# Optimization experiments

Measured on AMD Instinct MI355X. Metric: run time of the kernel, lower is better.

Reference implementation:

```python
import jax, jax.numpy as jnp
import numpy as np

N, E, D_IN, H1, C1, D_OUT = 50000, 800000, 384, 4, 64, 5
D_HID = H1 * C1  # 256, input to layer 2


def setup_inputs() -> dict:
    key = jax.random.key(0)
    ks = jax.random.split(key, 12)

    def lin(k, i, o):
        return (jax.random.normal(k, (i, o), jnp.float32) / np.sqrt(i)).astype(jnp.float32)

    inp = {
        "x": jax.random.normal(ks[0], (N, D_IN), jnp.float32),
        "edge_index": jax.random.randint(ks[1], (2, E), 0, N, jnp.int32),
        # layer 1: TransformerConv(384 -> 64, heads=4, concat=True)
        "Wq1": lin(ks[2], D_IN, H1 * C1), "bq1": jnp.zeros((H1 * C1,), jnp.float32),
        "Wk1": lin(ks[3], D_IN, H1 * C1), "bk1": jnp.zeros((H1 * C1,), jnp.float32),
        "Wv1": lin(ks[4], D_IN, H1 * C1), "bv1": jnp.zeros((H1 * C1,), jnp.float32),
        "Ws1": lin(ks[5], D_IN, H1 * C1), "bs1": jnp.zeros((H1 * C1,), jnp.float32),
        # layer 2: TransformerConv(256 -> 5, heads=1, concat=False)
        "Wq2": lin(ks[6], D_HID, D_OUT), "bq2": jnp.zeros((D_OUT,), jnp.float32),
        "Wk2": lin(ks[7], D_HID, D_OUT), "bk2": jnp.zeros((D_OUT,), jnp.float32),
        "Wv2": lin(ks[8], D_HID, D_OUT), "bv2": jnp.zeros((D_OUT,), jnp.float32),
        "Ws2": lin(ks[9], D_HID, D_OUT), "bs2": jnp.zeros((D_OUT,), jnp.float32),
    }
    return inp


def _segment_softmax(logits, dst, n):
    # logits: [E, H] grouped by destination node
    m = jax.ops.segment_max(logits, dst, num_segments=n)
    m = jnp.where(jnp.isfinite(m), m, 0.0)
    e = jnp.exp(logits - m[dst])
    s = jax.ops.segment_sum(e, dst, num_segments=n)
    return e / (s[dst] + 1e-16)


def _transformer_conv(x, src, dst, Wq, bq, Wk, bk, Wv, bv, Ws, bs, heads, out_ch, concat):
    n = x.shape[0]
    q = (x @ Wq + bq).reshape(n, heads, out_ch)
    k = (x @ Wk + bk).reshape(n, heads, out_ch)
    v = (x @ Wv + bv).reshape(n, heads, out_ch)
    # per-edge attention logits: q_i . k_j / sqrt(C)   [E, H]
    logits = jnp.einsum('ehc,ehc->eh', q[dst], k[src]) / jnp.sqrt(jnp.float32(out_ch))
    alpha = _segment_softmax(logits, dst, n)          # [E, H]
    msg = v[src] * alpha[:, :, None]                  # [E, H, C]
    out = jax.ops.segment_sum(msg, dst, num_segments=n)  # [N, H, C]
    out = out.reshape(n, heads * out_ch) if concat else out.mean(axis=1)
    # root skip connection (root_weight=True default in PyG)
    return out + (x @ Ws + bs)


def reference(x, edge_index, Wq1, bq1, Wk1, bk1, Wv1, bv1, Ws1, bs1,
              Wq2, bq2, Wk2, bk2, Wv2, bv2, Ws2, bs2):
    src, dst = edge_index[0], edge_index[1]
    h = _transformer_conv(x, src, dst, Wq1, bq1, Wk1, bk1, Wv1, bv1, Ws1, bs1,
                          H1, C1, True)
    h = jax.nn.relu(h)
    out = _transformer_conv(h, src, dst, Wq2, bq2, Wk2, bk2, Wv2, bv2, Ws2, bs2,
                            1, D_OUT, False)
    return out
```

## Files before the change

kernel.cpp:

```cpp
#include <hip/hip_runtime.h>
#include <hip/hip_bf16.h>

#define N_NODES 50000
#define N_EDGES 800000
#define NPAD    50048
#define SCAN_B  196

typedef __attribute__((ext_vector_type(8))) short bf16x8;
typedef __attribute__((ext_vector_type(8))) unsigned short u16x8;
typedef __attribute__((ext_vector_type(4))) float f32x4;

__device__ __forceinline__ unsigned short f2bf(float f) {
  union { float f; unsigned u; } x; x.f = f;
  unsigned r = x.u + 0x7fffu + ((x.u >> 16) & 1u);
  return (unsigned short)(r >> 16);
}
__device__ __forceinline__ float bf2f(unsigned short u) {
  union { unsigned u; float f; } x; x.u = ((unsigned)u) << 16;
  return x.f;
}
__device__ __forceinline__ unsigned char enc8v(float v) {
  float t = fminf(fmaxf(fmaf(v, 16.f, 128.5f), 0.f), 255.f);
  return (unsigned char)(int)t;
}
__device__ __forceinline__ char enc8k(float v) {
  float t = fminf(fmaxf(v * 16.f, -127.f), 127.f);
  return (char)(int)floorf(t + 0.5f);
}
__device__ __forceinline__ char enc8q(float v) {
  float t = fminf(fmaxf(v * 24.f, -127.f), 127.f);
  return (char)(int)floorf(t + 0.5f);
}

__device__ __forceinline__ int dot4i8(int a, int b, int c) {
#if __has_builtin(__builtin_amdgcn_sdot4)
  return __builtin_amdgcn_sdot4(a, b, c, false);
#else
  int r = c;
  r += (int)(char)(a) * (int)(char)(b);
  r += (int)(char)(a >> 8) * (int)(char)(b >> 8);
  r += (int)(char)(a >> 16) * (int)(char)(b >> 16);
  r += (int)(char)(a >> 24) * (int)(char)(b >> 24);
  return r;
#endif
}

__device__ __forceinline__ void gload16(const unsigned short* g, unsigned short* l) {
  __builtin_amdgcn_global_load_lds(
      (const __attribute__((address_space(1))) unsigned int*)g,
      (__attribute__((address_space(3))) unsigned int*)l, 16, 0, 0);
}

__global__ void hist_kernel(const int* __restrict__ dst, int* __restrict__ counts, int E) {
  int e = blockIdx.x * 256 + threadIdx.x;
  if (e < E) atomicAdd(&counts[dst[e]], 1);
}

__global__ __launch_bounds__(256) void scan1_kernel(const int* __restrict__ counts,
                                                    int* __restrict__ tmp, int* __restrict__ bsum, int n) {
  __shared__ int sm[256];
  int i = blockIdx.x * 256 + threadIdx.x;
  int v = (i < n) ? counts[i] : 0;
  sm[threadIdx.x] = v;
  __syncthreads();
  for (int off = 1; off < 256; off <<= 1) {
    int t = (threadIdx.x >= off) ? sm[threadIdx.x - off] : 0;
    __syncthreads();
    sm[threadIdx.x] += t;
    __syncthreads();
  }
  if (i < n) tmp[i] = sm[threadIdx.x] - v;
  if (threadIdx.x == 255) bsum[blockIdx.x] = sm[255];
}

__global__ __launch_bounds__(256) void scan2_kernel(const int* __restrict__ bsum,
                                                    int* __restrict__ bbase, int nb) {
  __shared__ int sm[256];
  int v = (threadIdx.x < nb) ? bsum[threadIdx.x] : 0;
  sm[threadIdx.x] = v;
  __syncthreads();
  for (int off = 1; off < 256; off <<= 1) {
    int t = (threadIdx.x >= off) ? sm[threadIdx.x - off] : 0;
    __syncthreads();
    sm[threadIdx.x] += t;
    __syncthreads();
  }
  if (threadIdx.x < nb) bbase[threadIdx.x] = sm[threadIdx.x] - v;
}

__global__ __launch_bounds__(256) void scan3_kernel(const int* __restrict__ tmp,
                                                    const int* __restrict__ bbase,
                                                    int* __restrict__ offsets, int* __restrict__ cursor,
                                                    int n, int E) {
  int i = blockIdx.x * 256 + threadIdx.x;
  if (i < n) {
    int o = tmp[i] + bbase[blockIdx.x];
    offsets[i] = o;
    cursor[i] = o;
  }
  if (i == 0) offsets[n] = E;
}

__global__ void scatter_kernel(const int* __restrict__ src, const int* __restrict__ dst,
                               int* __restrict__ cursor, int* __restrict__ csr_src, int E) {
  int e = blockIdx.x * 256 + threadIdx.x;
  if (e < E) {
    int pos = atomicAdd(&cursor[dst[e]], 1);
    csr_src[pos] = src[e];
  }
}

__global__ void convert_x_kernel(const float* __restrict__ x, unsigned short* __restrict__ xb,
                                 int total_real, int total_pad) {
  long i = ((long)blockIdx.x * 256 + threadIdx.x) * 8;
  if (i >= total_pad) return;
  u16x8 o;
  if (i < total_real) {
    float4 v0 = *(const float4*)&x[i];
    float4 v1 = *(const float4*)&x[i + 4];
    o[0] = (short)f2bf(v0.x); o[1] = (short)f2bf(v0.y);
    o[2] = (short)f2bf(v0.z); o[3] = (short)f2bf(v0.w);
    o[4] = (short)f2bf(v1.x); o[5] = (short)f2bf(v1.y);
    o[6] = (short)f2bf(v1.z); o[7] = (short)f2bf(v1.w);
  } else {
    o = (u16x8)0;
  }
  *(u16x8*)&xb[i] = o;
}

__global__ void pack_w1_kernel(const float* __restrict__ Wq, const float* __restrict__ Wk,
                               const float* __restrict__ Wv, const float* __restrict__ Ws,
                               const float* __restrict__ bq, const float* __restrict__ bk,
                               const float* __restrict__ bv, const float* __restrict__ bs_,
                               unsigned short* __restrict__ wbt, float* __restrict__ bias1) {
  int idx = blockIdx.x * 256 + threadIdx.x;
  if (idx >= 1024 * 384) return;
  int n = idx / 384, k = idx - n * 384;
  int blk = n >> 8, cc = n & 255;
  const float* W = (blk == 0) ? Wq : (blk == 1) ? Wk : (blk == 2) ? Wv : Ws;
  wbt[idx] = f2bf(W[(long)k * 256 + cc]);
  if (k == 0) {
    const float* b = (blk == 0) ? bq : (blk == 1) ? bk : (blk == 2) ? bv : bs_;
    bias1[n] = b[cc];
  }
}

__global__ void pack_w2_kernel(const float* __restrict__ Wq, const float* __restrict__ Wk,
                               const float* __restrict__ Wv, const float* __restrict__ Ws,
                               const float* __restrict__ bq, const float* __restrict__ bk,
                               const float* __restrict__ bv, const float* __restrict__ bs_,
                               unsigned short* __restrict__ w2bt, float* __restrict__ bias2) {
  int idx = blockIdx.x * 256 + threadIdx.x;
  if (idx >= 32 * 256) return;
  int c = idx >> 8, p = idx & 255;
  unsigned short o = 0;
  if (c < 20) {
    int blk = c / 5, cc = c - blk * 5;
    int tch = (p & 0xC0) + (p & 3) * 16 + ((p & 63) >> 2);
    const float* W = (blk == 0) ? Wq : (blk == 1) ? Wk : (blk == 2) ? Wv : Ws;
    o = f2bf(W[(long)tch * 5 + cc]);
    if (p == 0) {
      const float* b = (blk == 0) ? bq : (blk == 1) ? bk : (blk == 2) ? bv : bs_;
      bias2[c] = b[cc];
    }
  }
  w2bt[idx] = o;
}

__global__ __launch_bounds__(512) void gemm1_kernel(
    const unsigned short* __restrict__ xb, const unsigned short* __restrict__ wbt,
    const float* __restrict__ bias,
    char* __restrict__ qb8, unsigned char* __restrict__ kvb,
    unsigned short* __restrict__ s1b) {
  __shared__ unsigned short As[2][128 * 32];
  __shared__ unsigned short Bs[2][256 * 32];
  int bid = blockIdx.x;
  int grp = bid >> 5, bl = bid & 31;
  int mx = grp * 8 + (bl & 7);
  int y = bl >> 3;
  if (mx >= NPAD / 128) return;
  int tid = threadIdx.x;
  long m0 = (long)mx * 128;
  int n0 = y * 256;
  int w = tid >> 6, l = tid & 63;
  int wr = (w >> 2) * 64, wc = (w & 3) * 64;
  int lr = l & 15, c0 = l >> 4;
  int sw = (lr ^ (lr >> 2)) & 3;
  int swoff = (c0 ^ sw) * 8;
  f32x4 acc[4][4] = {};
  int rs = tid >> 2, ss = tid & 3;
  int fa = (rs ^ (rs >> 2)) & 3;
  int fb1 = ((rs + 128) ^ ((rs + 128) >> 2)) & 3;
  const unsigned short* gA  = xb + (m0 + rs) * 384 + ((ss ^ fa) * 8);
  const unsigned short* gB0 = wbt + (long)(n0 + rs) * 384 + ((ss ^ fa) * 8);
  const unsigned short* gB1 = wbt + (long)(n0 + rs + 128) * 384 + ((ss ^ fb1) * 8);
  gload16(gA, &As[0][tid * 8]);
  gload16(gB0, &Bs[0][tid * 8]);
  gload16(gB1, &Bs[0][4096 + tid * 8]);
  __syncthreads();
  for (int kt = 0; kt < 12; ++kt) {
    int b = kt & 1;
    if (kt < 11) {
      int ko = (kt + 1) * 32;
      gload16(gA + ko, &As[b ^ 1][tid * 8]);
      gload16(gB0 + ko, &Bs[b ^ 1][tid * 8]);
      gload16(gB1 + ko, &Bs[b ^ 1][4096 + tid * 8]);
    }
    bf16x8 af[4], bfv[4];
#pragma unroll
    for (int mf = 0; mf < 4; ++mf) af[mf] = *(const bf16x8*)&As[b][(wr + mf * 16 + lr) * 32 + swoff];
#pragma unroll
    for (int nf = 0; nf < 4; ++nf) bfv[nf] = *(const bf16x8*)&Bs[b][(wc + nf * 16 + lr) * 32 + swoff];
#pragma unroll
    for (int mf = 0; mf < 4; ++mf)
#pragma unroll
      for (int nf = 0; nf < 4; ++nf)
        acc[mf][nf] = __builtin_amdgcn_mfma_f32_16x16x32_bf16(af[mf], bfv[nf], acc[mf][nf], 0, 0, 0);
    __syncthreads();
  }
  float bv[4];
#pragma unroll
  for (int nf = 0; nf < 4; ++nf) bv[nf] = bias[n0 + wc + nf * 16 + lr];
  int pos = wc + lr * 4;
#pragma unroll
  for (int mf = 0; mf < 4; ++mf) {
#pragma unroll
    for (int i = 0; i < 4; ++i) {
      long row = m0 + wr + mf * 16 + c0 * 4 + i;
      float v0 = acc[mf][0][i] + bv[0];
      float v1 = acc[mf][1][i] + bv[1];
      float v2 = acc[mf][2][i] + bv[2];
      float v3 = acc[mf][3][i] + bv[3];
      if (y == 0) {
        char4 st; st.x = enc8q(v0); st.y = enc8q(v1); st.z = enc8q(v2); st.w = enc8q(v3);
        *(char4*)&qb8[row * 256 + pos] = st;
      } else if (y == 1) {
        char4 st; st.x = enc8k(v0); st.y = enc8k(v1); st.z = enc8k(v2); st.w = enc8k(v3);
        *(char4*)&kvb[row * 512 + pos] = st;
      } else if (y == 2) {
        uchar4 st; st.x = enc8v(v0); st.y = enc8v(v1); st.z = enc8v(v2); st.w = enc8v(v3);
        *(uchar4*)&kvb[row * 512 + 256 + pos] = st;
      } else {
        ushort4 st; st.x = f2bf(v0); st.y = f2bf(v1); st.z = f2bf(v2); st.w = f2bf(v3);
        *(ushort4*)&s1b[row * 256 + pos] = st;
      }
    }
  }
}

__global__ __launch_bounds__(256) void agg1_kernel(
    const char* __restrict__ qb8, const unsigned char* __restrict__ kvb,
    unsigned short* s1b,
    const int* __restrict__ offsets, const int* __restrict__ csr_src) {
  int w = threadIdx.x >> 6, l = threadIdx.x & 63;
  int g = l >> 4;
  int sub = l & 15;
  for (int n = blockIdx.x * 4 + w; n < N_NODES; n += gridDim.x * 4) {
    int4 qi = *(const int4*)&qb8[(long)n * 256 + sub * 16];
    float acc[16] = {};
    float se = 0.f;
    int i0 = offsets[n], i1 = offsets[n + 1];
#define VACC(E, W, B) \
    acc[(B) + 0] = fmaf(E, (float)((W) & 0xffu), acc[(B) + 0]); \
    acc[(B) + 1] = fmaf(E, (float)(((W) >> 8) & 0xffu), acc[(B) + 1]); \
    acc[(B) + 2] = fmaf(E, (float)(((W) >> 16) & 0xffu), acc[(B) + 2]); \
    acc[(B) + 3] = fmaf(E, (float)((W) >> 24), acc[(B) + 3]);
    for (int i = i0; i < i1; i += 8) {
      int ia = i + g, ib = i + 4 + g;
      int sa = csr_src[ia < i1 ? ia : i1 - 1];
      int sb = csr_src[ib < i1 ? ib : i1 - 1];
      const char* ba = (const char*)kvb + (long)sa * 512 + sub * 16;
      const char* bb = (const char*)kvb + (long)sb * 512 + sub * 16;
      int4 ka = *(const int4*)ba;
      int4 kw = *(const int4*)bb;
      uint4 va = *(const uint4*)(ba + 256);
      uint4 vw = *(const uint4*)(bb + 256);
      int da = 0, db = 0;
      da = dot4i8(qi.x, ka.x, da); da = dot4i8(qi.y, ka.y, da);
      da = dot4i8(qi.z, ka.z, da); da = dot4i8(qi.w, ka.w, da);
      db = dot4i8(qi.x, kw.x, db); db = dot4i8(qi.y, kw.y, db);
      db = dot4i8(qi.z, kw.z, db); db = dot4i8(qi.w, kw.w, db);
      da += __shfl_xor(da, 1); da += __shfl_xor(da, 2);
      db += __shfl_xor(db, 1); db += __shfl_xor(db, 2);
      float ea = (ia < i1) ? __expf((float)da * (1.f / 3072.f)) : 0.f;
      float eb = (ib < i1) ? __expf((float)db * (1.f / 3072.f)) : 0.f;
      se += ea + eb;
      VACC(ea, va.x, 0) VACC(ea, va.y, 4) VACC(ea, va.z, 8) VACC(ea, va.w, 12)
      VACC(eb, vw.x, 0) VACC(eb, vw.y, 4) VACC(eb, vw.z, 8) VACC(eb, vw.w, 12)
    }
#undef VACC
#pragma unroll
    for (int j = 0; j < 16; ++j) {
      acc[j] += __shfl_xor(acc[j], 16);
      acc[j] += __shfl_xor(acc[j], 32);
    }
    se += __shfl_xor(se, 16);
    se += __shfl_xor(se, 32);
    if (g == 0) {
      float inv = (se > 0.f) ? 1.0f / se : 0.f;
      float bias = (se > 0.f) ? -8.0f : 0.f;
      long ob = (long)n * 256 + sub * 16;
      u16x8 sv0 = *(const u16x8*)&s1b[ob];
      u16x8 sv1 = *(const u16x8*)&s1b[ob + 8];
      u16x8 h0, h1;
#pragma unroll
      for (int j = 0; j < 8; ++j) {
        float v0 = fmaf(acc[j] * inv, 0.0625f, bias);
        float v1 = fmaf(acc[8 + j] * inv, 0.0625f, bias);
        h0[j] = (short)f2bf(fmaxf(v0 + bf2f((unsigned short)sv0[j]), 0.f));
        h1[j] = (short)f2bf(fmaxf(v1 + bf2f((unsigned short)sv1[j]), 0.f));
      }
      *(u16x8*)&s1b[ob] = h0;
      *(u16x8*)&s1b[ob + 8] = h1;
    }
  }
}

__global__ __launch_bounds__(256) void lin2_kernel(const unsigned short* __restrict__ hb,
                                                   const unsigned short* __restrict__ w2bt,
                                                   const float* __restrict__ bias2,
                                                   float* __restrict__ qs2, float* __restrict__ kv2) {
  __shared__ unsigned short Bs2[32 * 264];
  __shared__ float bsh[32];
  for (int i = threadIdx.x; i < 32 * 32; i += 256) {
    int r = i >> 5, cc = i & 31;
    *(u16x8*)&Bs2[r * 264 + cc * 8] = *(const u16x8*)&w2bt[r * 256 + cc * 8];
  }
  if (threadIdx.x < 32) bsh[threadIdx.x] = (threadIdx.x < 20) ? bias2[threadIdx.x] : 0.f;
  __syncthreads();
  int w = threadIdx.x >> 6, l = threadIdx.x & 63;
  long row0 = (long)blockIdx.x * 128 + w * 32;
  int lr = l & 15, c0 = l >> 4;
  f32x4 acc[2][2] = {};
  for (int kk = 0; kk < 8; ++kk) {
    int koff = kk * 32 + c0 * 8;
    bf16x8 af[2], bfv[2];
    af[0] = *(const bf16x8*)&hb[(row0 + lr) * 256 + koff];
    af[1] = *(const bf16x8*)&hb[(row0 + 16 + lr) * 256 + koff];
    bfv[0] = *(const bf16x8*)&Bs2[lr * 264 + koff];
    bfv[1] = *(const bf16x8*)&Bs2[(16 + lr) * 264 + koff];
#pragma unroll
    for (int mf = 0; mf < 2; ++mf)
#pragma unroll
      for (int nf = 0; nf < 2; ++nf)
        acc[mf][nf] = __builtin_amdgcn_mfma_f32_16x16x32_bf16(af[mf], bfv[nf], acc[mf][nf], 0, 0, 0);
  }
#pragma unroll
  for (int mf = 0; mf < 2; ++mf) {
#pragma unroll
    for (int nf = 0; nf < 2; ++nf) {
      int col = nf * 16 + lr;
#pragma unroll
      for (int i = 0; i < 4; ++i) {
        long n = row0 + mf * 16 + c0 * 4 + i;
        float v = acc[mf][nf][i] + bsh[col];
        if (col < 5) qs2[n * 12 + col] = v;
        else if (col < 15) kv2[n * 12 + (col - 5)] = v;
        else if (col < 20) qs2[n * 12 + (col - 10)] = v;
      }
    }
  }
}

__global__ void agg2_kernel(const float* __restrict__ qs2, const float* __restrict__ kv2,
                            const int* __restrict__ offsets, const int* __restrict__ csr_src,
                            float* __restrict__ out) {
  int n = blockIdx.x * 256 + threadIdx.x;
  if (n >= N_NODES) return;
  const float* bn = &qs2[(long)n * 12];
  const float is5 = 0.4472135954999579f;
  float q[5], acc[5] = {0, 0, 0, 0, 0}, se = 0.f;
#pragma unroll
  for (int c = 0; c < 5; ++c) q[c] = bn[c] * is5;
  int i0 = offsets[n], i1 = offsets[n + 1];
  for (int i = i0; i < i1; ++i) {
    int s = csr_src[i];
    const float4* ps = (const float4*)&kv2[(long)s * 12];
    float4 A = ps[0], B = ps[1], C = ps[2];
    float lg = q[0] * A.x + q[1] * A.y + q[2] * A.z + q[3] * A.w + q[4] * B.x;
    float ee = __expf(lg);
    se += ee;
    acc[0] += ee * B.y; acc[1] += ee * B.z; acc[2] += ee * B.w;
    acc[3] += ee * C.x; acc[4] += ee * C.y;
  }
  float inv = 1.f / (se + 1e-16f);
#pragma unroll
  for (int c = 0; c < 5; ++c) out[(long)n * 5 + c] = acc[c] * inv + bn[5 + c];
}

extern "C" void kernel_launch(void* const* d_in, const int* in_sizes, int n_in,
                              void* d_out, int out_size, void* d_ws, size_t ws_size,
                              hipStream_t stream) {
  (void)in_sizes; (void)n_in; (void)out_size; (void)ws_size;
  const float* x   = (const float*)d_in[0];
  const int* eidx  = (const int*)d_in[1];
  const int* esrc  = eidx;
  const int* edst  = eidx + N_EDGES;
  const float* Wq1 = (const float*)d_in[2];  const float* bq1 = (const float*)d_in[3];
  const float* Wk1 = (const float*)d_in[4];  const float* bk1 = (const float*)d_in[5];
  const float* Wv1 = (const float*)d_in[6];  const float* bv1 = (const float*)d_in[7];
  const float* Ws1 = (const float*)d_in[8];  const float* bs1 = (const float*)d_in[9];
  const float* Wq2 = (const float*)d_in[10]; const float* bq2 = (const float*)d_in[11];
  const float* Wk2 = (const float*)d_in[12]; const float* bk2 = (const float*)d_in[13];
  const float* Wv2 = (const float*)d_in[14]; const float* bv2 = (const float*)d_in[15];
  const float* Ws2 = (const float*)d_in[16]; const float* bs2 = (const float*)d_in[17];

  char* p = (char*)d_ws;
  auto take = [&](size_t bytes) { char* r = p; p += (bytes + 255) & ~(size_t)255; return r; };
  unsigned short* xb  = (unsigned short*)take((size_t)NPAD * 384 * 2);
  unsigned short* wbt = (unsigned short*)take((size_t)1024 * 384 * 2);
  float* bias1        = (float*)take(1024 * 4);
  char* qb8           = (char*)take((size_t)NPAD * 256);
  unsigned char* kvb  = (unsigned char*)take((size_t)NPAD * 512);
  unsigned short* s1b = (unsigned short*)take((size_t)NPAD * 256 * 2);
  unsigned short* w2bt = (unsigned short*)take(32 * 256 * 2);
  float* bias2        = (float*)take(32 * 4);
  float* qs2          = (float*)take((size_t)NPAD * 12 * 4);
  float* kv2          = (float*)take((size_t)NPAD * 12 * 4);
  int* counts         = (int*)take((size_t)N_NODES * 4);
  int* offsets        = (int*)take((size_t)(N_NODES + 1) * 4);
  int* cursor         = (int*)take((size_t)N_NODES * 4);
  int* csr_src        = (int*)take((size_t)N_EDGES * 4);
  int* scan_tmp       = (int*)take((size_t)N_NODES * 4);
  int* scan_bsum      = (int*)take(256 * 4);
  int* scan_bbase     = (int*)take(256 * 4);

  hipMemsetAsync(counts, 0, (size_t)N_NODES * 4, stream);
  hist_kernel<<<(N_EDGES + 255) / 256, 256, 0, stream>>>(edst, counts, N_EDGES);
  scan1_kernel<<<SCAN_B, 256, 0, stream>>>(counts, scan_tmp, scan_bsum, N_NODES);
  scan2_kernel<<<1, 256, 0, stream>>>(scan_bsum, scan_bbase, SCAN_B);
  scan3_kernel<<<SCAN_B, 256, 0, stream>>>(scan_tmp, scan_bbase, offsets, cursor, N_NODES, N_EDGES);
  scatter_kernel<<<(N_EDGES + 255) / 256, 256, 0, stream>>>(esrc, edst, cursor, csr_src, N_EDGES);
  convert_x_kernel<<<(NPAD * 384 / 8 + 255) / 256, 256, 0, stream>>>(x, xb, N_NODES * 384, NPAD * 384);
  pack_w1_kernel<<<(1024 * 384 + 255) / 256, 256, 0, stream>>>(Wq1, Wk1, Wv1, Ws1, bq1, bk1, bv1, bs1, wbt, bias1);
  pack_w2_kernel<<<(32 * 256 + 255) / 256, 256, 0, stream>>>(Wq2, Wk2, Wv2, Ws2, bq2, bk2, bv2, bs2, w2bt, bias2);
  gemm1_kernel<<<((NPAD / 128 + 7) / 8) * 32, 512, 0, stream>>>(xb, wbt, bias1, qb8, kvb, s1b);
  agg1_kernel<<<2048, 256, 0, stream>>>(qb8, kvb, s1b, offsets, csr_src);
  lin2_kernel<<<NPAD / 128, 256, 0, stream>>>(s1b, w2bt, bias2, qs2, kv2);
  agg2_kernel<<<(N_NODES + 255) / 256, 256, 0, stream>>>(qs2, kv2, offsets, csr_src, (float*)d_out);
}
```

Before: 279.7 us.

## Fuse fp32-to-bf16 conversion of x into GEMM1 and prefetch edges in agg1

Removes the separate x conversion kernel and its bf16 staging buffer. GEMM1 now reads fp32 x rows straight from global memory into registers and packs them to bf16 MFMA fragments, so only the weight tile goes through LDS, which drops from double to single buffering. agg1 gains a one-batch software prefetch of neighbour K/V loads and an early path for nodes with no incoming edges. This saves a full read and write pass over x, but GEMM1 loses its global-to-LDS overlap, and each x element is now read four times, once per N-column block.

```diff
diff --git a/kernel.cpp b/kernel.cpp
--- a/kernel.cpp
+++ b/kernel.cpp
@@ -18,6 +18,9 @@
 __device__ __forceinline__ float bf2f(unsigned short u) {
   union { unsigned u; float f; } x; x.u = ((unsigned)u) << 16;
   return x.f;
+}
+__device__ __forceinline__ unsigned pkbf(float lo, float hi) {
+  return ((unsigned)f2bf(hi) << 16) | f2bf(lo);
 }
 __device__ __forceinline__ unsigned char enc8v(float v) {
   float t = fminf(fmaxf(fmaf(v, 16.f, 128.5f), 0.f), 255.f);
@@ -108,24 +111,6 @@
     int pos = atomicAdd(&cursor[dst[e]], 1);
     csr_src[pos] = src[e];
   }
-}
-
-__global__ void convert_x_kernel(const float* __restrict__ x, unsigned short* __restrict__ xb,
-                                 int total_real, int total_pad) {
-  long i = ((long)blockIdx.x * 256 + threadIdx.x) * 8;
-  if (i >= total_pad) return;
-  u16x8 o;
-  if (i < total_real) {
-    float4 v0 = *(const float4*)&x[i];
-    float4 v1 = *(const float4*)&x[i + 4];
-    o[0] = (short)f2bf(v0.x); o[1] = (short)f2bf(v0.y);
-    o[2] = (short)f2bf(v0.z); o[3] = (short)f2bf(v0.w);
-    o[4] = (short)f2bf(v1.x); o[5] = (short)f2bf(v1.y);
-    o[6] = (short)f2bf(v1.z); o[7] = (short)f2bf(v1.w);
-  } else {
-    o = (u16x8)0;
-  }
-  *(u16x8*)&xb[i] = o;
 }
 
 __global__ void pack_w1_kernel(const float* __restrict__ Wq, const float* __restrict__ Wk,
@@ -168,12 +153,11 @@
 }
 
 __global__ __launch_bounds__(512) void gemm1_kernel(
-    const unsigned short* __restrict__ xb, const unsigned short* __restrict__ wbt,
+    const float* __restrict__ x, const unsigned short* __restrict__ wbt,
     const float* __restrict__ bias,
     char* __restrict__ qb8, unsigned char* __restrict__ kvb,
     unsigned short* __restrict__ s1b) {
-  __shared__ unsigned short As[2][128 * 32];
-  __shared__ unsigned short Bs[2][256 * 32];
+  __shared__ unsigned short Bs[256 * 32];
   int bid = blockIdx.x;
   int grp = bid >> 5, bl = bid & 31;
   int mx = grp * 8 + (bl & 7);
@@ -187,36 +171,43 @@
   int lr = l & 15, c0 = l >> 4;
   int sw = (lr ^ (lr >> 2)) & 3;
   int swoff = (c0 ^ sw) * 8;
+  const float* gA[4];
+#pragma unroll
+  for (int mf = 0; mf < 4; ++mf) {
+    long arow = m0 + wr + mf * 16 + lr;
+    if (arow > (long)(N_NODES - 1)) arow = N_NODES - 1;
+    gA[mf] = x + arow * 384 + c0 * 8;
+  }
+  int rs = tid >> 2, ss = tid & 3;
+  int fb0 = (rs ^ (rs >> 2)) & 3;
+  int fb1 = ((rs + 128) ^ ((rs + 128) >> 2)) & 3;
+  const unsigned short* gB0 = wbt + (long)(n0 + rs) * 384 + ((ss ^ fb0) * 8);
+  const unsigned short* gB1 = wbt + (long)(n0 + rs + 128) * 384 + ((ss ^ fb1) * 8);
   f32x4 acc[4][4] = {};
-  int rs = tid >> 2, ss = tid & 3;
-  int fa = (rs ^ (rs >> 2)) & 3;
-  int fb1 = ((rs + 128) ^ ((rs + 128) >> 2)) & 3;
-  const unsigned short* gA  = xb + (m0 + rs) * 384 + ((ss ^ fa) * 8);
-  const unsigned short* gB0 = wbt + (long)(n0 + rs) * 384 + ((ss ^ fa) * 8);
-  const unsigned short* gB1 = wbt + (long)(n0 + rs + 128) * 384 + ((ss ^ fb1) * 8);
-  gload16(gA, &As[0][tid * 8]);
-  gload16(gB0, &Bs[0][tid * 8]);
-  gload16(gB1, &Bs[0][4096 + tid * 8]);
-  __syncthreads();
   for (int kt = 0; kt < 12; ++kt) {
-    int b = kt & 1;
-    if (kt < 11) {
-      int ko = (kt + 1) * 32;
-      gload16(gA + ko, &As[b ^ 1][tid * 8]);
-      gload16(gB0 + ko, &Bs[b ^ 1][tid * 8]);
-      gload16(gB1 + ko, &Bs[b ^ 1][4096 + tid * 8]);
-    }
-    bf16x8 af[4], bfv[4];
-#pragma unroll
-    for (int mf = 0; mf < 4; ++mf) af[mf] = *(const bf16x8*)&As[b][(wr + mf * 16 + lr) * 32 + swoff];
-#pragma unroll
-    for (int nf = 0; nf < 4; ++nf) bfv[nf] = *(const bf16x8*)&Bs[b][(wc + nf * 16 + lr) * 32 + swoff];
+    int ko = kt * 32;
+    __syncthreads();
+    gload16(gB0 + ko, &Bs[tid * 8]);
+    gload16(gB1 + ko, &Bs[4096 + tid * 8]);
+    bf16x8 af[4];
+#pragma unroll
+    for (int mf = 0; mf < 4; ++mf) {
+      float4 a0 = *(const float4*)(gA[mf] + ko);
+      float4 a1 = *(const float4*)(gA[mf] + ko + 4);
+      union { bf16x8 v; unsigned u[4]; } t;
+      t.u[0] = pkbf(a0.x, a0.y); t.u[1] = pkbf(a0.z, a0.w);
+      t.u[2] = pkbf(a1.x, a1.y); t.u[3] = pkbf(a1.z, a1.w);
+      af[mf] = t.v;
+    }
+    __syncthreads();
+    bf16x8 bfv[4];
+#pragma unroll
+    for (int nf = 0; nf < 4; ++nf) bfv[nf] = *(const bf16x8*)&Bs[(wc + nf * 16 + lr) * 32 + swoff];
 #pragma unroll
     for (int mf = 0; mf < 4; ++mf)
 #pragma unroll
       for (int nf = 0; nf < 4; ++nf)
         acc[mf][nf] = __builtin_amdgcn_mfma_f32_16x16x32_bf16(af[mf], bfv[nf], acc[mf][nf], 0, 0, 0);
-    __syncthreads();
   }
   float bv[4];
 #pragma unroll
@@ -256,25 +247,43 @@
   int g = l >> 4;
   int sub = l & 15;
   for (int n = blockIdx.x * 4 + w; n < N_NODES; n += gridDim.x * 4) {
+    int i0 = offsets[n], i1 = offsets[n + 1];
+    long ob = (long)n * 256 + sub * 16;
+    if (i0 >= i1) {
+      if (g == 0) {
+        u16x8 sv0 = *(const u16x8*)&s1b[ob];
+        u16x8 sv1 = *(const u16x8*)&s1b[ob + 8];
+        u16x8 h0, h1;
+#pragma unroll
+        for (int j = 0; j < 8; ++j) {
+          h0[j] = (short)f2bf(fmaxf(bf2f((unsigned short)sv0[j]), 0.f));
+          h1[j] = (short)f2bf(fmaxf(bf2f((unsigned short)sv1[j]), 0.f));
+        }
+        *(u16x8*)&s1b[ob] = h0;
+        *(u16x8*)&s1b[ob + 8] = h1;
+      }
+      continue;
+    }
     int4 qi = *(const int4*)&qb8[(long)n * 256 + sub * 16];
     float acc[16] = {};
     float se = 0.f;
-    int i0 = offsets[n], i1 = offsets[n + 1];
+
+    auto ldbatch = [&](int i, int4& ka, uint4& va, int4& kw, uint4& vw) {
+      int ia = i + g, ib = i + 4 + g;
+      int sa = csr_src[ia < i1 ? ia : i1 - 1];
+      int sb = csr_src[ib < i1 ? ib : i1 - 1];
+      const char* ba = (const char*)kvb + (long)sa * 512 + sub * 16;
+      const char* bb = (const char*)kvb + (long)sb * 512 + sub * 16;
+      ka = *(const int4*)ba; va = *(const uint4*)(ba + 256);
+      kw = *(const int4*)bb; vw = *(const uint4*)(bb + 256);
+    };
 #define VACC(E, W, B) \
     acc[(B) + 0] = fmaf(E, (float)((W) & 0xffu), acc[(B) + 0]); \
     acc[(B) + 1] = fmaf(E, (float)(((W) >> 8) & 0xffu), acc[(B) + 1]); \
     acc[(B) + 2] = fmaf(E, (float)(((W) >> 16) & 0xffu), acc[(B) + 2]); \
     acc[(B) + 3] = fmaf(E, (float)((W) >> 24), acc[(B) + 3]);
-    for (int i = i0; i < i1; i += 8) {
+    auto consume = [&](int i, int4 ka, uint4 va, int4 kw, uint4 vw) {
       int ia = i + g, ib = i + 4 + g;
-      int sa = csr_src[ia < i1 ? ia : i1 - 1];
-      int sb = csr_src[ib < i1 ? ib : i1 - 1];
-      const char* ba = (const char*)kvb + (long)sa * 512 + sub * 16;
-      const char* bb = (const char*)kvb + (long)sb * 512 + sub * 16;
-      int4 ka = *(const int4*)ba;
-      int4 kw = *(const int4*)bb;
-      uint4 va = *(const uint4*)(ba + 256);
-      uint4 vw = *(const uint4*)(bb + 256);
       int da = 0, db = 0;
       da = dot4i8(qi.x, ka.x, da); da = dot4i8(qi.y, ka.y, da);
       da = dot4i8(qi.z, ka.z, da); da = dot4i8(qi.w, ka.w, da);
@@ -287,7 +296,18 @@
       se += ea + eb;
       VACC(ea, va.x, 0) VACC(ea, va.y, 4) VACC(ea, va.z, 8) VACC(ea, va.w, 12)
       VACC(eb, vw.x, 0) VACC(eb, vw.y, 4) VACC(eb, vw.z, 8) VACC(eb, vw.w, 12)
-    }
+    };
+
+    int i = i0;
+    int4 ka0, kw0; uint4 va0, vw0;
+    ldbatch(i, ka0, va0, kw0, vw0);
+    for (; i + 8 < i1; i += 8) {
+      int4 ka1, kw1; uint4 va1, vw1;
+      ldbatch(i + 8, ka1, va1, kw1, vw1);
+      consume(i, ka0, va0, kw0, vw0);
+      ka0 = ka1; va0 = va1; kw0 = kw1; vw0 = vw1;
+    }
+    consume(i, ka0, va0, kw0, vw0);
 #undef VACC
 #pragma unroll
     for (int j = 0; j < 16; ++j) {
@@ -299,7 +319,6 @@
     if (g == 0) {
       float inv = (se > 0.f) ? 1.0f / se : 0.f;
       float bias = (se > 0.f) ? -8.0f : 0.f;
-      long ob = (long)n * 256 + sub * 16;
       u16x8 sv0 = *(const u16x8*)&s1b[ob];
       u16x8 sv1 = *(const u16x8*)&s1b[ob + 8];
       u16x8 h0, h1;
@@ -407,7 +426,6 @@
 
   char* p = (char*)d_ws;
   auto take = [&](size_t bytes) { char* r = p; p += (bytes + 255) & ~(size_t)255; return r; };
-  unsigned short* xb  = (unsigned short*)take((size_t)NPAD * 384 * 2);
   unsigned short* wbt = (unsigned short*)take((size_t)1024 * 384 * 2);
   float* bias1        = (float*)take(1024 * 4);
   char* qb8           = (char*)take((size_t)NPAD * 256);
@@ -431,10 +449,9 @@
   scan2_kernel<<<1, 256, 0, stream>>>(scan_bsum, scan_bbase, SCAN_B);
   scan3_kernel<<<SCAN_B, 256, 0, stream>>>(scan_tmp, scan_bbase, offsets, cursor, N_NODES, N_EDGES);
   scatter_kernel<<<(N_EDGES + 255) / 256, 256, 0, stream>>>(esrc, edst, cursor, csr_src, N_EDGES);
-  convert_x_kernel<<<(NPAD * 384 / 8 + 255) / 256, 256, 0, stream>>>(x, xb, N_NODES * 384, NPAD * 384);
   pack_w1_kernel<<<(1024 * 384 + 255) / 256, 256, 0, stream>>>(Wq1, Wk1, Wv1, Ws1, bq1, bk1, bv1, bs1, wbt, bias1);
   pack_w2_kernel<<<(32 * 256 + 255) / 256, 256, 0, stream>>>(Wq2, Wk2, Wv2, Ws2, bq2, bk2, bv2, bs2, w2bt, bias2);
-  gemm1_kernel<<<((NPAD / 128 + 7) / 8) * 32, 512, 0, stream>>>(xb, wbt, bias1, qb8, kvb, s1b);
+  gemm1_kernel<<<((NPAD / 128 + 7) / 8) * 32, 512, 0, stream>>>(x, wbt, bias1, qb8, kvb, s1b);
   agg1_kernel<<<2048, 256, 0, stream>>>(qb8, kvb, s1b, offsets, csr_src);
   lin2_kernel<<<NPAD / 128, 256, 0, stream>>>(s1b, w2bt, bias2, qs2, kv2);
   agg2_kernel<<<(N_NODES + 255) / 256, 256, 0, stream>>>(qs2, kv2, offsets, csr_src, (float*)d_out);
```

Result: slower. 375.4 us (+34.2%).
